# Kernel tuning notes

Measured on AMD Instinct MI355X. Metric: run time of the kernel, lower is better.

## Reference

```python
import jax, jax.numpy as jnp
import numpy as np

LEVELS = 16
FEATURES = 2
HASHMAP_SIZE = 524288
BASE_RES = 16
PER_LEVEL_SCALE = 1.3819

_P1, _P2, _P3 = np.uint32(73856093), np.uint32(19349663), np.uint32(83492791)
# 8 trilinear corner offsets, bit order (x, y, z)
_OFFSETS = np.array([[ox, oy, oz] for ox in (0, 1) for oy in (0, 1) for oz in (0, 1)], dtype=np.int32)


def setup_inputs() -> dict:
    key = jax.random.key(0)
    kx, kt = jax.random.split(key)
    x = jax.random.uniform(kx, (2000000, 3), dtype=jnp.float32)
    tables = jax.random.normal(kt, (LEVELS, HASHMAP_SIZE, FEATURES), dtype=jnp.float32) * 0.01
    return {"x": x, "tables": tables}


def _hash_coords(corners_u32):
    # corners_u32: [N, 8, 3] uint32; spatial hash with uint32 wraparound.
    h = (corners_u32[..., 0] * _P1) ^ (corners_u32[..., 1] * _P2) ^ (corners_u32[..., 2] * _P3)
    return (h % np.uint32(HASHMAP_SIZE)).astype(jnp.int32)  # [N, 8]


def _encode(x, tables):
    offsets_i = jnp.asarray(_OFFSETS)                 # [8, 3] int32
    offsets_f = offsets_i.astype(x.dtype)             # [8, 3]
    embeds = []
    for l in range(LEVELS):
        res = int(BASE_RES * PER_LEVEL_SCALE ** l)
        pos = x * res                                  # [N, 3]
        pos_floor = jnp.floor(pos)
        w = pos - pos_floor                            # [N, 3] trilinear weights
        base = pos_floor.astype(jnp.int32)             # non-negative (x in [0,1])
        corners = (base[:, None, :] + offsets_i).astype(jnp.uint32)  # [N, 8, 3]
        idx = _hash_coords(corners)                    # [N, 8]
        vals = tables[l][idx]                          # [N, 8, F] gather
        # weight per corner = prod over axes of (w if offset else 1-w)
        wgt = jnp.prod(offsets_f * w[:, None, :] + (1.0 - offsets_f) * (1.0 - w[:, None, :]), axis=-1)  # [N, 8]
        embeds.append(jnp.einsum('nc,ncf->nf', wgt, vals))  # [N, F]
    return jnp.concatenate(embeds, axis=-1)           # [N, LEVELS*F]


def reference(x, tables):
    return _encode(x, tables)
```

## Files before the change

kernel.cpp:

```cpp
#include <hip/hip_runtime.h>
#include <stdint.h>

#define LEVELS 16
#define FEAT 2
#define TABLE_SIZE 524288
#define TMASK (TABLE_SIZE - 1)

typedef float f32x2 __attribute__((ext_vector_type(2)));
typedef float f32x4 __attribute__((ext_vector_type(4)));
typedef float f32x4u __attribute__((ext_vector_type(4), aligned(8)));

__device__ __constant__ int kRes[LEVELS] = {
    16, 22, 30, 42, 58, 80, 111, 153, 212, 294, 406, 561, 775, 1072, 1481, 2047
};

#define P1 73856093u
#define P2 19349663u
#define P3 83492791u

#define D0 17
#define N0 4913
#define D1 23
#define N1 12167
#define SLAB 8192

#define D2 31
#define N2 29791
#define D3 43
#define N3 79507
#define D4 59
#define N4 205379
#define NDENSE (N2 + N3 + N4)

__global__ __launch_bounds__(256) void remap_kernel(
    const float* __restrict__ tables,
    f32x2* __restrict__ dense)
{
    const int d = blockIdx.x * 256 + threadIdx.x;
    if (d >= NDENSE) return;
    int l, D, rel;
    if (d < N2)            { l = 2; D = D2; rel = d; }
    else if (d < N2 + N3)  { l = 3; D = D3; rel = d - N2; }
    else                   { l = 4; D = D4; rel = d - N2 - N3; }
    const uint32_t bx = rel / (D * D);
    const uint32_t r  = rel - bx * (D * D);
    const uint32_t by = r / D;
    const uint32_t bz = r - by * D;
    const uint32_t slot = ((bx * P1) ^ (by * P2) ^ (bz * P3)) & TMASK;
    const f32x2* __restrict__ tab = reinterpret_cast<const f32x2*>(tables) + (size_t)l * TABLE_SIZE;
    dense[d] = tab[slot];
}

__global__ __launch_bounds__(256) void encode_low_kernel(
    const float* __restrict__ x,
    const float* __restrict__ tables,
    f32x2* __restrict__ ws,
    int n)
{
    __shared__ f32x2 tl[N0 + N1];
    __shared__ float sxc[256 * 3];
    const int t = threadIdx.x;

    const f32x2* __restrict__ tab0 = reinterpret_cast<const f32x2*>(tables);
    const f32x2* __restrict__ tab1 = tab0 + TABLE_SIZE;
    for (int d = t; d < N0; d += 256) {
        const uint32_t bx = d / (D0 * D0);
        const uint32_t r  = d - bx * (D0 * D0);
        const uint32_t by = r / D0;
        const uint32_t bz = r - by * D0;
        tl[d] = tab0[((bx * P1) ^ (by * P2) ^ (bz * P3)) & TMASK];
    }
    for (int d = t; d < N1; d += 256) {
        const uint32_t bx = d / (D1 * D1);
        const uint32_t r  = d - bx * (D1 * D1);
        const uint32_t by = r / D1;
        const uint32_t bz = r - by * D1;
        tl[N0 + d] = tab1[((bx * P1) ^ (by * P2) ^ (bz * P3)) & TMASK];
    }

    const int slab0 = blockIdx.x * SLAB;
    const long long total3 = (long long)n * 3;

    for (int chunk = 0; chunk < SLAB / 256; ++chunk) {
        const int p0 = slab0 + chunk * 256;
        if (p0 >= n) break;
        __syncthreads();
#pragma unroll
        for (int k = 0; k < 3; ++k) {
            const long long g = (long long)p0 * 3 + k * 256 + t;
            sxc[k * 256 + t] = (g < total3) ? __builtin_nontemporal_load(x + g) : 0.0f;
        }
        __syncthreads();

        const int i = p0 + t;
        if (i >= n) continue;
        const float px = sxc[3 * t + 0];
        const float py = sxc[3 * t + 1];
        const float pz = sxc[3 * t + 2];

        {
            const float fx = px * 16.0f, fy = py * 16.0f, fz = pz * 16.0f;
            const float flx = floorf(fx), fly = floorf(fy), flz = floorf(fz);
            const float wx = fx - flx, wy = fy - fly, wz = fz - flz;
            const float ux = 1.0f - wx, uy = 1.0f - wy, uz = 1.0f - wz;
            const int base = ((int)flx * D0 + (int)fly) * D0 + (int)flz;
            float f0 = 0.0f, f1 = 0.0f;
#pragma unroll
            for (int c = 0; c < 8; ++c) {
                const int off = ((c & 4) ? D0 * D0 : 0) + ((c & 2) ? D0 : 0) + (c & 1);
                const f32x2 v = tl[base + off];
                const float w = ((c & 4) ? wx : ux) * ((c & 2) ? wy : uy) * ((c & 1) ? wz : uz);
                f0 = fmaf(w, v.x, f0);
                f1 = fmaf(w, v.y, f1);
            }
            f32x2 r; r.x = f0; r.y = f1;
            __builtin_nontemporal_store(r, ws + i);
        }
        {
            const float fx = px * 22.0f, fy = py * 22.0f, fz = pz * 22.0f;
            const float flx = floorf(fx), fly = floorf(fy), flz = floorf(fz);
            const float wx = fx - flx, wy = fy - fly, wz = fz - flz;
            const float ux = 1.0f - wx, uy = 1.0f - wy, uz = 1.0f - wz;
            const int base = ((int)flx * D1 + (int)fly) * D1 + (int)flz + N0;
            float f0 = 0.0f, f1 = 0.0f;
#pragma unroll
            for (int c = 0; c < 8; ++c) {
                const int off = ((c & 4) ? D1 * D1 : 0) + ((c & 2) ? D1 : 0) + (c & 1);
                const f32x2 v = tl[base + off];
                const float w = ((c & 4) ? wx : ux) * ((c & 2) ? wy : uy) * ((c & 1) ? wz : uz);
                f0 = fmaf(w, v.x, f0);
                f1 = fmaf(w, v.y, f1);
            }
            f32x2 r; r.x = f0; r.y = f1;
            __builtin_nontemporal_store(r, ws + (size_t)n + i);
        }
    }
}

__device__ __constant__ int   kMidD[3]    = { D2, D3, D4 };
__device__ __constant__ int   kMidOff[3]  = { 0, N2, N2 + N3 };
__device__ __constant__ float kMidRes[3]  = { 30.0f, 42.0f, 58.0f };

__global__ __launch_bounds__(256) void encode_mid_kernel(
    const float* __restrict__ x,
    const f32x2* __restrict__ dense,
    f32x2* __restrict__ ws,
    int n, int nb)
{
    const int lsel = blockIdx.x / nb;
    const int blk  = blockIdx.x - lsel * nb;
    const int t    = threadIdx.x;
    const int p0   = blk * 512;

    __shared__ float sx[512 * 3];
    const long long total3 = (long long)n * 3;
    const long long gbase  = (long long)p0 * 3;
#pragma unroll
    for (int k = 0; k < 6; ++k) {
        long long g = gbase + k * 256 + t;
        sx[k * 256 + t] = (g < total3) ? __builtin_nontemporal_load(x + g) : 0.0f;
    }
    __syncthreads();

    const int   D    = kMidD[lsel];
    const float resf = kMidRes[lsel];
    const f32x2* __restrict__ tabd = dense + kMidOff[lsel];

    int   base[2];
    float wxa[2], wya[2], wza[2];
#pragma unroll
    for (int s = 0; s < 2; ++s) {
        const int tp = s * 256 + t;
        const float fx = sx[3 * tp + 0] * resf;
        const float fy = sx[3 * tp + 1] * resf;
        const float fz = sx[3 * tp + 2] * resf;
        const float flx = floorf(fx), fly = floorf(fy), flz = floorf(fz);
        wxa[s] = fx - flx; wya[s] = fy - fly; wza[s] = fz - flz;
        base[s] = ((int)flx * D + (int)fly) * D + (int)flz;
    }

    f32x4u v[2][4];
#pragma unroll
    for (int s = 0; s < 2; ++s)
#pragma unroll
        for (int p = 0; p < 4; ++p) {
            const int off = ((p & 2) ? D * D : 0) + ((p & 1) ? D : 0);
            v[s][p] = *reinterpret_cast<const f32x4u*>(tabd + base[s] + off);
        }

#pragma unroll
    for (int s = 0; s < 2; ++s) {
        const float wx = wxa[s], wy = wya[s], wz = wza[s];
        const float ux = 1.0f - wx, uy = 1.0f - wy, uz = 1.0f - wz;
        float f0 = 0.0f, f1 = 0.0f;
#pragma unroll
        for (int p = 0; p < 4; ++p) {
            const float wxy = ((p & 2) ? wx : ux) * ((p & 1) ? wy : uy);
            f0 = fmaf(wxy, fmaf(uz, v[s][p].x, wz * v[s][p].z), f0);
            f1 = fmaf(wxy, fmaf(uz, v[s][p].y, wz * v[s][p].w), f1);
        }
        const int i = p0 + s * 256 + t;
        if (i < n) {
            f32x2 r; r.x = f0; r.y = f1;
            __builtin_nontemporal_store(r, ws + (size_t)(2 + lsel) * n + i);
        }
    }
}

__global__ __launch_bounds__(256) void encode_level_kernel(
    const float* __restrict__ x,
    const float* __restrict__ tables,
    f32x2* __restrict__ ws,
    int n, int nb)
{
    const int l   = 5 + blockIdx.x / nb;
    const int blk = blockIdx.x - (l - 5) * nb;
    const int t   = threadIdx.x;
    const int p0  = blk * 512;

    __shared__ float sx[512 * 3];
    const long long total3 = (long long)n * 3;
    const long long gbase  = (long long)p0 * 3;
#pragma unroll
    for (int k = 0; k < 6; ++k) {
        long long g = gbase + k * 256 + t;
        sx[k * 256 + t] = (g < total3) ? __builtin_nontemporal_load(x + g) : 0.0f;
    }
    __syncthreads();

    const float resf = (float)kRes[l];
    const f32x2* __restrict__ tab = reinterpret_cast<const f32x2*>(tables) + (size_t)l * TABLE_SIZE;

    uint32_t idx[2][8];
    float    wgt[2][8];
#pragma unroll
    for (int s = 0; s < 2; ++s) {
        const int tp = s * 256 + t;
        const float fx = sx[3 * tp + 0] * resf;
        const float fy = sx[3 * tp + 1] * resf;
        const float fz = sx[3 * tp + 2] * resf;
        const float flx = floorf(fx), fly = floorf(fy), flz = floorf(fz);
        const float wx = fx - flx, wy = fy - fly, wz = fz - flz;
        const float ux = 1.0f - wx, uy = 1.0f - wy, uz = 1.0f - wz;
        const uint32_t hx0 = (uint32_t)(int)flx * P1, hx1 = hx0 + P1;
        const uint32_t hy0 = (uint32_t)(int)fly * P2, hy1 = hy0 + P2;
        const uint32_t hz0 = (uint32_t)(int)flz * P3, hz1 = hz0 + P3;
#pragma unroll
        for (int c = 0; c < 8; ++c) {
            const uint32_t hx = (c & 4) ? hx1 : hx0;
            const uint32_t hy = (c & 2) ? hy1 : hy0;
            const uint32_t hz = (c & 1) ? hz1 : hz0;
            idx[s][c] = (hx ^ hy ^ hz) & TMASK;
            wgt[s][c] = ((c & 4) ? wx : ux) * ((c & 2) ? wy : uy) * ((c & 1) ? wz : uz);
        }
    }

    f32x2 v[2][8];
#pragma unroll
    for (int s = 0; s < 2; ++s)
#pragma unroll
        for (int c = 0; c < 8; ++c)
            v[s][c] = tab[idx[s][c]];

#pragma unroll
    for (int s = 0; s < 2; ++s) {
        float f0 = 0.0f, f1 = 0.0f;
#pragma unroll
        for (int c = 0; c < 8; ++c) {
            f0 = fmaf(wgt[s][c], v[s][c].x, f0);
            f1 = fmaf(wgt[s][c], v[s][c].y, f1);
        }
        const int i = p0 + s * 256 + t;
        if (i < n) {
            f32x2 r; r.x = f0; r.y = f1;
            __builtin_nontemporal_store(r, ws + (size_t)l * n + i);
        }
    }
}

__global__ __launch_bounds__(256) void transpose_kernel(
    const f32x2* __restrict__ ws,
    float* __restrict__ out,
    int n)
{
    __shared__ float s[256 * 33];
    const int t  = threadIdx.x;
    const int p0 = blockIdx.x * 256;
    const int m  = min(256, n - p0);

    if (t < m) {
#pragma unroll
        for (int l = 0; l < LEVELS; ++l) {
            const f32x2 e = __builtin_nontemporal_load(ws + (size_t)l * n + p0 + t);
            s[t * 33 + 2 * l + 0] = e.x;
            s[t * 33 + 2 * l + 1] = e.y;
        }
    }
    __syncthreads();

    const int nchunk = m * 8;
    f32x4* __restrict__ o4 = reinterpret_cast<f32x4*>(out) + (size_t)p0 * 8;
#pragma unroll
    for (int j = 0; j < 8; ++j) {
        const int cl = j * 256 + t;
        if (cl < nchunk) {
            const int p = cl >> 3, ch = cl & 7;
            f32x4 q;
            q.x = s[p * 33 + ch * 4 + 0];
            q.y = s[p * 33 + ch * 4 + 1];
            q.z = s[p * 33 + ch * 4 + 2];
            q.w = s[p * 33 + ch * 4 + 3];
            __builtin_nontemporal_store(q, o4 + cl);
        }
    }
}

__global__ __launch_bounds__(256) void hashgrid_enc_kernel(
    const float* __restrict__ x,
    const float* __restrict__ tables,
    float* __restrict__ out,
    int n)
{
    __shared__ float sx[256 * 3];
    const int t = threadIdx.x;
    const int block0 = blockIdx.x * 256;
    const long long total3 = (long long)n * 3;
    const long long gbase = (long long)block0 * 3;
#pragma unroll
    for (int k = 0; k < 3; ++k) {
        long long g = gbase + k * 256 + t;
        sx[k * 256 + t] = (g < total3) ? x[g] : 0.0f;
    }
    __syncthreads();
    const int i = block0 + t;
    if (i >= n) return;
    const float px = sx[3 * t + 0];
    const float py = sx[3 * t + 1];
    const float pz = sx[3 * t + 2];
    float outv[2 * LEVELS];
#pragma unroll
    for (int l = 0; l < LEVELS; ++l) {
        const float resf = (float)kRes[l];
        const float fx = px * resf, fy = py * resf, fz = pz * resf;
        const float flx = floorf(fx), fly = floorf(fy), flz = floorf(fz);
        const float wx = fx - flx, wy = fy - fly, wz = fz - flz;
        const float ux = 1.0f - wx, uy = 1.0f - wy, uz = 1.0f - wz;
        const uint32_t hx0 = (uint32_t)(int)flx * P1, hx1 = hx0 + P1;
        const uint32_t hy0 = (uint32_t)(int)fly * P2, hy1 = hy0 + P2;
        const uint32_t hz0 = (uint32_t)(int)flz * P3, hz1 = hz0 + P3;
        const float* __restrict__ tab = tables + (size_t)l * (TABLE_SIZE * FEAT);
        float f0 = 0.0f, f1 = 0.0f;
#pragma unroll
        for (int c = 0; c < 8; ++c) {
            const uint32_t hx = (c & 4) ? hx1 : hx0;
            const uint32_t hy = (c & 2) ? hy1 : hy0;
            const uint32_t hz = (c & 1) ? hz1 : hz0;
            const uint32_t idx = (hx ^ hy ^ hz) & TMASK;
            const float2 v = *reinterpret_cast<const float2*>(tab + (size_t)idx * FEAT);
            const float w = ((c & 4) ? wx : ux) * ((c & 2) ? wy : uy) * ((c & 1) ? wz : uz);
            f0 = fmaf(w, v.x, f0);
            f1 = fmaf(w, v.y, f1);
        }
        outv[2 * l + 0] = f0;
        outv[2 * l + 1] = f1;
    }
    float4* __restrict__ o4 = reinterpret_cast<float4*>(out + (size_t)i * (2 * LEVELS));
#pragma unroll
    for (int k = 0; k < 8; ++k) {
        o4[k] = make_float4(outv[4 * k + 0], outv[4 * k + 1],
                            outv[4 * k + 2], outv[4 * k + 3]);
    }
}

extern "C" void kernel_launch(void* const* d_in, const int* in_sizes, int n_in,
                              void* d_out, int out_size, void* d_ws, size_t ws_size,
                              hipStream_t stream) {
    const float* x = (const float*)d_in[0];
    const float* tables = (const float*)d_in[1];
    float* out = (float*)d_out;
    const int n = in_sizes[0] / 3;

    const size_t ws_elems  = (size_t)LEVELS * (size_t)n;
    const size_t ws_needed = (ws_elems + NDENSE + 2) * sizeof(f32x2);
    if (ws_size >= ws_needed) {
        f32x2* ws    = (f32x2*)d_ws;
        f32x2* dense = ws + ws_elems;

        hipLaunchKernelGGL(remap_kernel, dim3((NDENSE + 255) / 256), dim3(256), 0, stream,
                           tables, dense);

        const int nspec = (n + SLAB - 1) / SLAB;
        hipLaunchKernelGGL(encode_low_kernel, dim3(nspec), dim3(256), 0, stream,
                           x, tables, ws, n);

        const int nb512 = (n + 511) / 512;
        hipLaunchKernelGGL(encode_mid_kernel, dim3(nb512 * 3), dim3(256), 0, stream,
                           x, dense, ws, n, nb512);
        hipLaunchKernelGGL(encode_level_kernel, dim3(nb512 * 11), dim3(256), 0, stream,
                           x, tables, ws, n, nb512);

        const int nb256 = (n + 255) / 256;
        hipLaunchKernelGGL(transpose_kernel, dim3(nb256), dim3(256), 0, stream,
                           ws, out, n);
    } else {
        const int nb = (n + 255) / 256;
        hipLaunchKernelGGL(hashgrid_enc_kernel, dim3(nb), dim3(256), 0, stream,
                           x, tables, out, n);
    }
}
```

Measured before the change: 1.094 ms.

## Fold low levels into dense-remap path and double points per thread

Levels 0 and 1 no longer use a separate kernel that keeps the table in LDS. They are remapped into the global dense table and handled by the generalized dense kernel, so one launch and the per-block LDS table fill go away. Both the dense and hashed kernels now process 4 points per thread (1024 per block), which puts more gathers in flight, and a sched_barrier keeps all loads issued before the math. In the hashed kernel the weights are recomputed after the gathers instead of being held in registers. The cost is higher register pressure, which may lower occupancy, and the levels 0/1 lookups move from LDS to the global/L2 path.

After: 1.126 ms. 2.9% more time.

```diff
diff --git a/kernel.cpp b/kernel.cpp
--- a/kernel.cpp
+++ b/kernel.cpp
@@ -22,15 +22,13 @@
 #define N0 4913
 #define D1 23
 #define N1 12167
-#define SLAB 8192
-
 #define D2 31
 #define N2 29791
 #define D3 43
 #define N3 79507
 #define D4 59
 #define N4 205379
-#define NDENSE (N2 + N3 + N4)
+#define NDENSE (N0 + N1 + N2 + N3 + N4)
 
 __global__ __launch_bounds__(256) void remap_kernel(
     const float* __restrict__ tables,
@@ -39,9 +37,11 @@
     const int d = blockIdx.x * 256 + threadIdx.x;
     if (d >= NDENSE) return;
     int l, D, rel;
-    if (d < N2)            { l = 2; D = D2; rel = d; }
-    else if (d < N2 + N3)  { l = 3; D = D3; rel = d - N2; }
-    else                   { l = 4; D = D4; rel = d - N2 - N3; }
+    if (d < N0)                          { l = 0; D = D0; rel = d; }
+    else if (d < N0 + N1)                { l = 1; D = D1; rel = d - N0; }
+    else if (d < N0 + N1 + N2)           { l = 2; D = D2; rel = d - N0 - N1; }
+    else if (d < N0 + N1 + N2 + N3)      { l = 3; D = D3; rel = d - N0 - N1 - N2; }
+    else                                 { l = 4; D = D4; rel = d - N0 - N1 - N2 - N3; }
     const uint32_t bx = rel / (D * D);
     const uint32_t r  = rel - bx * (D * D);
     const uint32_t by = r / D;
@@ -51,97 +51,11 @@
     dense[d] = tab[slot];
 }
 
-__global__ __launch_bounds__(256) void encode_low_kernel(
-    const float* __restrict__ x,
-    const float* __restrict__ tables,
-    f32x2* __restrict__ ws,
-    int n)
-{
-    __shared__ f32x2 tl[N0 + N1];
-    __shared__ float sxc[256 * 3];
-    const int t = threadIdx.x;
-
-    const f32x2* __restrict__ tab0 = reinterpret_cast<const f32x2*>(tables);
-    const f32x2* __restrict__ tab1 = tab0 + TABLE_SIZE;
-    for (int d = t; d < N0; d += 256) {
-        const uint32_t bx = d / (D0 * D0);
-        const uint32_t r  = d - bx * (D0 * D0);
-        const uint32_t by = r / D0;
-        const uint32_t bz = r - by * D0;
-        tl[d] = tab0[((bx * P1) ^ (by * P2) ^ (bz * P3)) & TMASK];
-    }
-    for (int d = t; d < N1; d += 256) {
-        const uint32_t bx = d / (D1 * D1);
-        const uint32_t r  = d - bx * (D1 * D1);
-        const uint32_t by = r / D1;
-        const uint32_t bz = r - by * D1;
-        tl[N0 + d] = tab1[((bx * P1) ^ (by * P2) ^ (bz * P3)) & TMASK];
-    }
-
-    const int slab0 = blockIdx.x * SLAB;
-    const long long total3 = (long long)n * 3;
-
-    for (int chunk = 0; chunk < SLAB / 256; ++chunk) {
-        const int p0 = slab0 + chunk * 256;
-        if (p0 >= n) break;
-        __syncthreads();
-#pragma unroll
-        for (int k = 0; k < 3; ++k) {
-            const long long g = (long long)p0 * 3 + k * 256 + t;
-            sxc[k * 256 + t] = (g < total3) ? __builtin_nontemporal_load(x + g) : 0.0f;
-        }
-        __syncthreads();
-
-        const int i = p0 + t;
-        if (i >= n) continue;
-        const float px = sxc[3 * t + 0];
-        const float py = sxc[3 * t + 1];
-        const float pz = sxc[3 * t + 2];
-
-        {
-            const float fx = px * 16.0f, fy = py * 16.0f, fz = pz * 16.0f;
-            const float flx = floorf(fx), fly = floorf(fy), flz = floorf(fz);
-            const float wx = fx - flx, wy = fy - fly, wz = fz - flz;
-            const float ux = 1.0f - wx, uy = 1.0f - wy, uz = 1.0f - wz;
-            const int base = ((int)flx * D0 + (int)fly) * D0 + (int)flz;
-            float f0 = 0.0f, f1 = 0.0f;
-#pragma unroll
-            for (int c = 0; c < 8; ++c) {
-                const int off = ((c & 4) ? D0 * D0 : 0) + ((c & 2) ? D0 : 0) + (c & 1);
-                const f32x2 v = tl[base + off];
-                const float w = ((c & 4) ? wx : ux) * ((c & 2) ? wy : uy) * ((c & 1) ? wz : uz);
-                f0 = fmaf(w, v.x, f0);
-                f1 = fmaf(w, v.y, f1);
-            }
-            f32x2 r; r.x = f0; r.y = f1;
-            __builtin_nontemporal_store(r, ws + i);
-        }
-        {
-            const float fx = px * 22.0f, fy = py * 22.0f, fz = pz * 22.0f;
-            const float flx = floorf(fx), fly = floorf(fy), flz = floorf(fz);
-            const float wx = fx - flx, wy = fy - fly, wz = fz - flz;
-            const float ux = 1.0f - wx, uy = 1.0f - wy, uz = 1.0f - wz;
-            const int base = ((int)flx * D1 + (int)fly) * D1 + (int)flz + N0;
-            float f0 = 0.0f, f1 = 0.0f;
-#pragma unroll
-            for (int c = 0; c < 8; ++c) {
-                const int off = ((c & 4) ? D1 * D1 : 0) + ((c & 2) ? D1 : 0) + (c & 1);
-                const f32x2 v = tl[base + off];
-                const float w = ((c & 4) ? wx : ux) * ((c & 2) ? wy : uy) * ((c & 1) ? wz : uz);
-                f0 = fmaf(w, v.x, f0);
-                f1 = fmaf(w, v.y, f1);
-            }
-            f32x2 r; r.x = f0; r.y = f1;
-            __builtin_nontemporal_store(r, ws + (size_t)n + i);
-        }
-    }
-}
-
-__device__ __constant__ int   kMidD[3]    = { D2, D3, D4 };
-__device__ __constant__ int   kMidOff[3]  = { 0, N2, N2 + N3 };
-__device__ __constant__ float kMidRes[3]  = { 30.0f, 42.0f, 58.0f };
-
-__global__ __launch_bounds__(256) void encode_mid_kernel(
+__device__ __constant__ int   kDD[5]    = { D0, D1, D2, D3, D4 };
+__device__ __constant__ int   kDOff[5]  = { 0, N0, N0 + N1, N0 + N1 + N2, N0 + N1 + N2 + N3 };
+__device__ __constant__ float kDRes[5]  = { 16.0f, 22.0f, 30.0f, 42.0f, 58.0f };
+
+__global__ __launch_bounds__(256) void encode_dense_kernel(
     const float* __restrict__ x,
     const f32x2* __restrict__ dense,
     f32x2* __restrict__ ws,
@@ -150,26 +64,27 @@
     const int lsel = blockIdx.x / nb;
     const int blk  = blockIdx.x - lsel * nb;
     const int t    = threadIdx.x;
-    const int p0   = blk * 512;
-
-    __shared__ float sx[512 * 3];
+    const int p0   = blk * 1024;
+
+    __shared__ float sx[1024 * 3];
     const long long total3 = (long long)n * 3;
     const long long gbase  = (long long)p0 * 3;
 #pragma unroll
-    for (int k = 0; k < 6; ++k) {
+    for (int k = 0; k < 12; ++k) {
         long long g = gbase + k * 256 + t;
         sx[k * 256 + t] = (g < total3) ? __builtin_nontemporal_load(x + g) : 0.0f;
     }
     __syncthreads();
 
-    const int   D    = kMidD[lsel];
-    const float resf = kMidRes[lsel];
-    const f32x2* __restrict__ tabd = dense + kMidOff[lsel];
-
-    int   base[2];
-    float wxa[2], wya[2], wza[2];
-#pragma unroll
-    for (int s = 0; s < 2; ++s) {
+    const int   D    = kDD[lsel];
+    const int   DD   = D * D;
+    const float resf = kDRes[lsel];
+    const f32x2* __restrict__ tabd = dense + kDOff[lsel];
+
+    int   base[4];
+    float wxa[4], wya[4], wza[4];
+#pragma unroll
+    for (int s = 0; s < 4; ++s) {
         const int tp = s * 256 + t;
         const float fx = sx[3 * tp + 0] * resf;
         const float fy = sx[3 * tp + 1] * resf;
@@ -179,17 +94,18 @@
         base[s] = ((int)flx * D + (int)fly) * D + (int)flz;
     }
 
-    f32x4u v[2][4];
-#pragma unroll
-    for (int s = 0; s < 2; ++s)
+    f32x4u v[4][4];
+#pragma unroll
+    for (int s = 0; s < 4; ++s)
 #pragma unroll
         for (int p = 0; p < 4; ++p) {
-            const int off = ((p & 2) ? D * D : 0) + ((p & 1) ? D : 0);
+            const int off = ((p & 2) ? DD : 0) + ((p & 1) ? D : 0);
             v[s][p] = *reinterpret_cast<const f32x4u*>(tabd + base[s] + off);
         }
-
-#pragma unroll
-    for (int s = 0; s < 2; ++s) {
+    __builtin_amdgcn_sched_barrier(0);
+
+#pragma unroll
+    for (int s = 0; s < 4; ++s) {
         const float wx = wxa[s], wy = wya[s], wz = wza[s];
         const float ux = 1.0f - wx, uy = 1.0f - wy, uz = 1.0f - wz;
         float f0 = 0.0f, f1 = 0.0f;
@@ -202,7 +118,7 @@
         const int i = p0 + s * 256 + t;
         if (i < n) {
             f32x2 r; r.x = f0; r.y = f1;
-            __builtin_nontemporal_store(r, ws + (size_t)(2 + lsel) * n + i);
+            __builtin_nontemporal_store(r, ws + (size_t)lsel * n + i);
         }
     }
 }
@@ -216,13 +132,13 @@
     const int l   = 5 + blockIdx.x / nb;
     const int blk = blockIdx.x - (l - 5) * nb;
     const int t   = threadIdx.x;
-    const int p0  = blk * 512;
-
-    __shared__ float sx[512 * 3];
+    const int p0  = blk * 1024;
+
+    __shared__ float sx[1024 * 3];
     const long long total3 = (long long)n * 3;
     const long long gbase  = (long long)p0 * 3;
 #pragma unroll
-    for (int k = 0; k < 6; ++k) {
+    for (int k = 0; k < 12; ++k) {
         long long g = gbase + k * 256 + t;
         sx[k * 256 + t] = (g < total3) ? __builtin_nontemporal_load(x + g) : 0.0f;
     }
@@ -231,17 +147,16 @@
     const float resf = (float)kRes[l];
     const f32x2* __restrict__ tab = reinterpret_cast<const f32x2*>(tables) + (size_t)l * TABLE_SIZE;
 
-    uint32_t idx[2][8];
-    float    wgt[2][8];
-#pragma unroll
-    for (int s = 0; s < 2; ++s) {
+    uint32_t idx[4][8];
+    float    wxa[4], wya[4], wza[4];
+#pragma unroll
+    for (int s = 0; s < 4; ++s) {
         const int tp = s * 256 + t;
         const float fx = sx[3 * tp + 0] * resf;
         const float fy = sx[3 * tp + 1] * resf;
         const float fz = sx[3 * tp + 2] * resf;
         const float flx = floorf(fx), fly = floorf(fy), flz = floorf(fz);
-        const float wx = fx - flx, wy = fy - fly, wz = fz - flz;
-        const float ux = 1.0f - wx, uy = 1.0f - wy, uz = 1.0f - wz;
+        wxa[s] = fx - flx; wya[s] = fy - fly; wza[s] = fz - flz;
         const uint32_t hx0 = (uint32_t)(int)flx * P1, hx1 = hx0 + P1;
         const uint32_t hy0 = (uint32_t)(int)fly * P2, hy1 = hy0 + P2;
         const uint32_t hz0 = (uint32_t)(int)flz * P3, hz1 = hz0 + P3;
@@ -251,24 +166,27 @@
             const uint32_t hy = (c & 2) ? hy1 : hy0;
             const uint32_t hz = (c & 1) ? hz1 : hz0;
             idx[s][c] = (hx ^ hy ^ hz) & TMASK;
-            wgt[s][c] = ((c & 4) ? wx : ux) * ((c & 2) ? wy : uy) * ((c & 1) ? wz : uz);
-        }
-    }
-
-    f32x2 v[2][8];
-#pragma unroll
-    for (int s = 0; s < 2; ++s)
+        }
+    }
+
+    f32x2 v[4][8];
+#pragma unroll
+    for (int s = 0; s < 4; ++s)
 #pragma unroll
         for (int c = 0; c < 8; ++c)
             v[s][c] = tab[idx[s][c]];
-
-#pragma unroll
-    for (int s = 0; s < 2; ++s) {
+    __builtin_amdgcn_sched_barrier(0);
+
+#pragma unroll
+    for (int s = 0; s < 4; ++s) {
+        const float wx = wxa[s], wy = wya[s], wz = wza[s];
+        const float ux = 1.0f - wx, uy = 1.0f - wy, uz = 1.0f - wz;
         float f0 = 0.0f, f1 = 0.0f;
 #pragma unroll
         for (int c = 0; c < 8; ++c) {
-            f0 = fmaf(wgt[s][c], v[s][c].x, f0);
-            f1 = fmaf(wgt[s][c], v[s][c].y, f1);
+            const float w = ((c & 4) ? wx : ux) * ((c & 2) ? wy : uy) * ((c & 1) ? wz : uz);
+            f0 = fmaf(w, v[s][c].x, f0);
+            f1 = fmaf(w, v[s][c].y, f1);
         }
         const int i = p0 + s * 256 + t;
         if (i < n) {
@@ -389,15 +307,11 @@
         hipLaunchKernelGGL(remap_kernel, dim3((NDENSE + 255) / 256), dim3(256), 0, stream,
                            tables, dense);
 
-        const int nspec = (n + SLAB - 1) / SLAB;
-        hipLaunchKernelGGL(encode_low_kernel, dim3(nspec), dim3(256), 0, stream,
-                           x, tables, ws, n);
-
-        const int nb512 = (n + 511) / 512;
-        hipLaunchKernelGGL(encode_mid_kernel, dim3(nb512 * 3), dim3(256), 0, stream,
-                           x, dense, ws, n, nb512);
-        hipLaunchKernelGGL(encode_level_kernel, dim3(nb512 * 11), dim3(256), 0, stream,
-                           x, tables, ws, n, nb512);
+        const int nb1024 = (n + 1023) / 1024;
+        hipLaunchKernelGGL(encode_dense_kernel, dim3(nb1024 * 5), dim3(256), 0, stream,
+                           x, dense, ws, n, nb1024);
+        hipLaunchKernelGGL(encode_level_kernel, dim3(nb1024 * 11), dim3(256), 0, stream,
+                           x, tables, ws, n, nb1024);
 
         const int nb256 = (n + 255) / 256;
         hipLaunchKernelGGL(transpose_kernel, dim3(nb256), dim3(256), 0, stream,
```
